# Kernel optimization log

Measured on AMD Instinct MI355X. Metric: run time of the kernel, lower is better.

The kernel has to match this reference:

```python
import jax, jax.numpy as jnp
import numpy as np

NUM_HEADS = 16


def setup_inputs() -> dict:
    key = jax.random.key(0)
    k1, k2, k3 = jax.random.split(key, 3)
    T, B, E = 2048, 2, 1024
    x = jax.random.normal(k1, (T, B, E), dtype=jnp.float32)
    in_proj_w = jax.random.normal(k2, (E, 3 * E), dtype=jnp.float32) * (E ** -0.5)
    in_proj_b = jnp.zeros((3 * E,), dtype=jnp.float32)
    out_w = jax.random.normal(k3, (E, E), dtype=jnp.float32) * (E ** -0.5)
    out_b = jnp.zeros((E,), dtype=jnp.float32)
    return {"x": x, "in_proj_w": in_proj_w, "in_proj_b": in_proj_b,
            "out_w": out_w, "out_b": out_b}


def reference(x, in_proj_w, in_proj_b, out_w, out_b):
    # x: (tgt_len, bsz, embed_dim) -- seq-first, self-attention (q is k is v)
    T, B, E = x.shape
    H = NUM_HEADS
    D = E // H
    scaling = D ** -0.5
    # packed in-projection: einsum('bne,ef->bnf') over (T,B,E)
    proj = jnp.einsum('tbe,ef->tbf', x, in_proj_w) + in_proj_b
    q, k, v = jnp.split(proj, 3, axis=-1)  # each (T, B, E)
    # reshape to (T, B*H, D) then transpose to (B*H, T, D)
    q = q.reshape(T, B * H, D).transpose(1, 0, 2)
    k = k.reshape(T, B * H, D).transpose(1, 0, 2)
    v = v.reshape(T, B * H, D).transpose(1, 0, 2)
    # full O(T^2) attention matrix, scaling applied after QK^T as in source
    attn = jnp.einsum('bie,bje->bij', q, k) * scaling  # (B*H, T, T)
    attn = jax.nn.softmax(attn, axis=-1)
    out = jnp.einsum('bij,bje->bie', attn, v)  # (B*H, T, D)
    # faithful to source: reshape directly (no head transpose-back)
    out = out.reshape(B, T, E)
    out = jnp.einsum('bte,ef->btf', out, out_w) + out_b
    return out
```

## Files before the change

### kernel.cpp

```cpp
#include <hip/hip_runtime.h>
#include <stdint.h>

#define TSEQ 2048
#define NB 2
#define EMB 1024
#define NHEAD 16
#define HDIM 64
#define KSPLIT 4
#define NT (TSEQ / KSPLIT / 64)
#define QSCALE 0.18033688f

typedef __bf16 bf16x8 __attribute__((ext_vector_type(8)));
typedef __bf16 bf16x4 __attribute__((ext_vector_type(4)));
typedef float f32x4 __attribute__((ext_vector_type(4)));

__device__ __forceinline__ void gload_lds16(const void* g, void* lds) {
    __builtin_amdgcn_global_load_lds(
        (const __attribute__((address_space(1))) unsigned int*)g,
        (__attribute__((address_space(3))) unsigned int*)lds, 16, 0, 0);
}

__global__ __launch_bounds__(256) void cvt_x_kernel(
    const float* __restrict__ x, __bf16* __restrict__ xb)
{
    const size_t idx = ((size_t)blockIdx.x * 256 + threadIdx.x) * 4;
    float4 v = *(const float4*)(x + idx);
    bf16x4 o = { (__bf16)v.x, (__bf16)v.y, (__bf16)v.z, (__bf16)v.w };
    *(bf16x4*)(xb + idx) = o;
}

__global__ __launch_bounds__(256) void transpose_cvt_kernel(
    const float* __restrict__ w_in, const float* __restrict__ w_out,
    __bf16* __restrict__ wiT, __bf16* __restrict__ whT)
{
    __shared__ float tile[32][33];
    int bx = blockIdx.x;
    const int by = blockIdx.y;
    const float* src; __bf16* dst; int sn;
    if (bx < 96) { src = w_in;  dst = wiT; sn = 3072; }
    else         { bx -= 96; src = w_out; dst = whT; sn = 1024; }
    const int tx = threadIdx.x, ty = threadIdx.y;
    #pragma unroll
    for (int i = 0; i < 4; ++i)
        tile[ty + i * 8][tx] = src[(size_t)(by * 32 + ty + i * 8) * sn + bx * 32 + tx];
    __syncthreads();
    #pragma unroll
    for (int i = 0; i < 4; ++i) {
        float v = tile[tx][ty + i * 8];
        dst[(size_t)(bx * 32 + ty + i * 8) * 1024 + by * 32 + tx] = (__bf16)v;
    }
}

__global__ __launch_bounds__(256) void gemm_qkv_kernel(
    const __bf16* __restrict__ A, const __bf16* __restrict__ BT,
    const float* __restrict__ bias,
    __bf16* __restrict__ Oq, __bf16* __restrict__ Ok, __bf16* __restrict__ Ov)
{
    __shared__ __align__(16) __bf16 As[128 * 64];
    __shared__ __align__(16) __bf16 Bs[128 * 64];
    const int tid = threadIdx.x;
    const int wave = tid >> 6, lane = tid & 63;
    const int l16 = lane & 15, quad = lane >> 4;
    const int wm = wave >> 1, wn = wave & 1;
    const int m0 = blockIdx.y * 128, n0 = blockIdx.x * 128;

    f32x4 acc[4][4];
    #pragma unroll
    for (int mt = 0; mt < 4; ++mt)
        #pragma unroll
        for (int nt = 0; nt < 4; ++nt)
            #pragma unroll
            for (int r = 0; r < 4; ++r) acc[mt][nt][r] = 0.f;

    int smrow[4], schunk[4], sbase[4];
    #pragma unroll
    for (int i = 0; i < 4; ++i) {
        int linear = (wave * 4 + i) * 64 + lane;
        smrow[i] = linear >> 3;
        schunk[i] = (linear & 7) ^ (smrow[i] & 7);
        sbase[i] = (wave * 4 + i) * 512;
    }

    for (int k0 = 0; k0 < 1024; k0 += 64) {
        #pragma unroll
        for (int i = 0; i < 4; ++i) {
            gload_lds16(A + (size_t)(m0 + smrow[i]) * 1024 + k0 + schunk[i] * 8,
                        As + sbase[i]);
            gload_lds16(BT + (size_t)(n0 + smrow[i]) * 1024 + k0 + schunk[i] * 8,
                        Bs + sbase[i]);
        }
        __syncthreads();
        #pragma unroll
        for (int kk = 0; kk < 2; ++kk) {
            bf16x8 am[4], bn[4];
            #pragma unroll
            for (int mt = 0; mt < 4; ++mt) {
                int row = wm * 64 + mt * 16 + l16;
                int c = (kk * 4 + quad) ^ (row & 7);
                am[mt] = *(const bf16x8*)(As + row * 64 + c * 8);
            }
            #pragma unroll
            for (int nt = 0; nt < 4; ++nt) {
                int row = wn * 64 + nt * 16 + l16;
                int c = (kk * 4 + quad) ^ (row & 7);
                bn[nt] = *(const bf16x8*)(Bs + row * 64 + c * 8);
            }
            #pragma unroll
            for (int mt = 0; mt < 4; ++mt)
                #pragma unroll
                for (int nt = 0; nt < 4; ++nt)
                    acc[mt][nt] = __builtin_amdgcn_mfma_f32_16x16x32_bf16(
                        am[mt], bn[nt], acc[mt][nt], 0, 0, 0);
        }
        __syncthreads();
    }

    #pragma unroll
    for (int nt = 0; nt < 4; ++nt) {
        const int col = n0 + wn * 64 + nt * 16 + l16;
        const float bv = bias[col];
        const int sec = col >> 10, f = col & 1023;
        const int h = f >> 6, d = f & 63;
        #pragma unroll
        for (int mt = 0; mt < 4; ++mt)
            #pragma unroll
            for (int r = 0; r < 4; ++r) {
                const int row = m0 + wm * 64 + mt * 16 + quad * 4 + r;
                float v = acc[mt][nt][r] + bv;
                const int t = row >> 1, b = row & 1;
                const int bh = b * NHEAD + h;
                if (sec == 0)
                    Oq[((size_t)bh * TSEQ + t) * HDIM + d] = (__bf16)(v * QSCALE);
                else if (sec == 1)
                    Ok[((size_t)bh * TSEQ + t) * HDIM + d] = (__bf16)v;
                else
                    Ov[((size_t)bh * HDIM + d) * TSEQ + t] = (__bf16)v;
            }
    }
}

__global__ __launch_bounds__(256, 4) void attn_mfma_kernel(
    const __bf16* __restrict__ Q, const __bf16* __restrict__ K,
    const __bf16* __restrict__ Vt,
    __bf16* __restrict__ O0, __bf16* __restrict__ O1,
    __bf16* __restrict__ O2, __bf16* __restrict__ O3,
    float* __restrict__ L0, float* __restrict__ L1,
    float* __restrict__ L2, float* __restrict__ L3)
{
    __shared__ __align__(16) __bf16 Ks[64 * 64];
    __shared__ __align__(16) __bf16 Vs[2][64 * 64];
    __shared__ __align__(16) __bf16 Ps[4][32 * 64];

    const int tid  = threadIdx.x;
    const int wave = tid >> 6;
    const int lane = tid & 63;
    const int l16  = lane & 15;
    const int quad = lane >> 4;
    const int bh   = blockIdx.y;
    const int z    = blockIdx.z;
    const int q0   = blockIdx.x * 128 + wave * 32;
    const int kbase0 = z * (TSEQ / KSPLIT);

    __bf16* __restrict__ Opart = (z == 0) ? O0 : (z == 1) ? O1 : (z == 2) ? O2 : O3;
    float*  __restrict__ Lpart = (z == 0) ? L0 : (z == 1) ? L1 : (z == 2) ? L2 : L3;

    bf16x8 qf[2][2];
    #pragma unroll
    for (int mq = 0; mq < 2; ++mq) {
        const __bf16* Qrow = Q + ((size_t)bh * TSEQ + q0 + mq * 16 + l16) * HDIM;
        qf[mq][0] = *(const bf16x8*)(Qrow + quad * 8);
        qf[mq][1] = *(const bf16x8*)(Qrow + 32 + quad * 8);
    }

    f32x4 Oacc[2][4];
    #pragma unroll
    for (int mq = 0; mq < 2; ++mq)
        #pragma unroll
        for (int dt = 0; dt < 4; ++dt)
            #pragma unroll
            for (int r = 0; r < 4; ++r) Oacc[mq][dt][r] = 0.f;
    float l_part[2] = {0.f, 0.f};

    const __bf16* Kbase = K + ((size_t)bh * TSEQ + kbase0) * HDIM;
    const __bf16* Vbase = Vt + (size_t)bh * HDIM * TSEQ + kbase0;

    int srow[2], schk[2];
    #pragma unroll
    for (int i = 0; i < 2; ++i) {
        const int s = wave * 2 + i;
        srow[i] = s * 8 + (lane >> 3);
        schk[i] = (lane & 7) ^ (srow[i] & 7);
    }

#define STAGE(buf, kt)                                                        \
    {                                                                         \
        _Pragma("unroll")                                                     \
        for (int i = 0; i < 2; ++i) {                                         \
            const int s = wave * 2 + i;                                       \
            gload_lds16(Kbase + (size_t)((kt) * 64 + srow[i]) * HDIM          \
                            + schk[i] * 8,                                    \
                        Ks + s * 512);                                        \
            gload_lds16(Vbase + (size_t)srow[i] * TSEQ + (kt) * 64            \
                            + schk[i] * 8,                                    \
                        &Vs[buf][s * 512]);                                   \
        }                                                                     \
    }

    STAGE(0, 0);

    for (int kt = 0; kt < NT; ++kt) {
        const int buf = kt & 1;
        __syncthreads();

        bf16x8 kf[4][2];
        #pragma unroll
        for (int nt = 0; nt < 4; ++nt) {
            const int row = nt * 16 + l16;
            #pragma unroll
            for (int ch = 0; ch < 2; ++ch) {
                const int c = (quad + 4 * ch) ^ (row & 7);
                kf[nt][ch] = *(const bf16x8*)(&Ks[row * 64 + c * 8]);
            }
        }
        __syncthreads();
        if (kt + 1 < NT) STAGE(buf ^ 1, kt + 1);

        #pragma unroll
        for (int mq = 0; mq < 2; ++mq) {
            #pragma unroll
            for (int nt = 0; nt < 4; ++nt) {
                f32x4 s = {0.f, 0.f, 0.f, 0.f};
                s = __builtin_amdgcn_mfma_f32_16x16x32_bf16(kf[nt][0], qf[mq][0], s, 0, 0, 0);
                s = __builtin_amdgcn_mfma_f32_16x16x32_bf16(kf[nt][1], qf[mq][1], s, 0, 0, 0);
                float p0 = exp2f(s[0]), p1 = exp2f(s[1]);
                float p2 = exp2f(s[2]), p3 = exp2f(s[3]);
                l_part[mq] += (p0 + p1) + (p2 + p3);
                bf16x4 pk = { (__bf16)p0, (__bf16)p1, (__bf16)p2, (__bf16)p3 };
                const int prow = mq * 16 + l16;
                const int kidx = nt * 16 + quad * 4;
                const int pos = ((kidx >> 3) ^ (prow & 7)) * 8 + (kidx & 7);
                *(bf16x4*)(&Ps[wave][prow * 64 + pos]) = pk;
            }
        }

        bf16x8 pa[2][2];
        #pragma unroll
        for (int mq = 0; mq < 2; ++mq) {
            const int prow = mq * 16 + l16;
            #pragma unroll
            for (int h = 0; h < 2; ++h) {
                const int c = (quad + 4 * h) ^ (prow & 7);
                pa[mq][h] = *(const bf16x8*)(&Ps[wave][prow * 64 + c * 8]);
            }
        }
        #pragma unroll
        for (int dt = 0; dt < 4; ++dt) {
            const int row = dt * 16 + l16;
            bf16x8 v0, v1;
            {
                const int c0 = quad ^ (row & 7);
                const int c1 = (quad + 4) ^ (row & 7);
                v0 = *(const bf16x8*)(&Vs[buf][row * 64 + c0 * 8]);
                v1 = *(const bf16x8*)(&Vs[buf][row * 64 + c1 * 8]);
            }
            #pragma unroll
            for (int mq = 0; mq < 2; ++mq) {
                Oacc[mq][dt] = __builtin_amdgcn_mfma_f32_16x16x32_bf16(
                    pa[mq][0], v0, Oacc[mq][dt], 0, 0, 0);
                Oacc[mq][dt] = __builtin_amdgcn_mfma_f32_16x16x32_bf16(
                    pa[mq][1], v1, Oacc[mq][dt], 0, 0, 0);
            }
        }
    }
#undef STAGE

    #pragma unroll
    for (int mq = 0; mq < 2; ++mq) {
        float v = l_part[mq];
        v += __shfl_xor(v, 16);
        v += __shfl_xor(v, 32);
        if (quad == 0)
            Lpart[(size_t)bh * TSEQ + q0 + mq * 16 + l16] = v;
    }

    const size_t base = ((size_t)bh * TSEQ + q0) * HDIM;
    #pragma unroll
    for (int mq = 0; mq < 2; ++mq)
        #pragma unroll
        for (int dt = 0; dt < 4; ++dt)
            #pragma unroll
            for (int r = 0; r < 4; ++r) {
                const size_t idx = base +
                    (size_t)(mq * 16 + quad * 4 + r) * HDIM + dt * 16 + l16;
                Opart[idx] = (__bf16)Oacc[mq][dt][r];
            }
}

__global__ __launch_bounds__(256) void normalize_kernel(
    const __bf16* __restrict__ O0, const __bf16* __restrict__ O1,
    const __bf16* __restrict__ O2, const __bf16* __restrict__ O3,
    const float* __restrict__ L0, const float* __restrict__ L1,
    const float* __restrict__ L2, const float* __restrict__ L3,
    __bf16* __restrict__ Ob)
{
    const size_t gid = (size_t)blockIdx.x * 256 + threadIdx.x;
    const size_t idx = gid * 8;
    const size_t qi = idx >> 6;
    const float inv = 1.f / (L0[qi] + L1[qi] + L2[qi] + L3[qi]);
    bf16x8 a = *(const bf16x8*)(O0 + idx);
    bf16x8 b = *(const bf16x8*)(O1 + idx);
    bf16x8 c = *(const bf16x8*)(O2 + idx);
    bf16x8 d = *(const bf16x8*)(O3 + idx);
    bf16x8 o;
    #pragma unroll
    for (int j = 0; j < 8; ++j)
        o[j] = (__bf16)((((float)a[j] + (float)b[j]) +
                         ((float)c[j] + (float)d[j])) * inv);
    *(bf16x8*)(Ob + idx) = o;
}

__global__ __launch_bounds__(256) void gemm_out_kernel(
    const __bf16* __restrict__ A, const __bf16* __restrict__ BT,
    const float* __restrict__ bias, float* __restrict__ out)
{
    __shared__ __align__(16) __bf16 As[64 * 64];
    __shared__ __align__(16) __bf16 Bs[64 * 64];
    const int tid = threadIdx.x;
    const int wave = tid >> 6, lane = tid & 63;
    const int l16 = lane & 15, quad = lane >> 4;
    const int wm = wave >> 1, wn = wave & 1;
    const int m0 = blockIdx.y * 64, n0 = blockIdx.x * 64;

    f32x4 acc[2][2];
    #pragma unroll
    for (int mt = 0; mt < 2; ++mt)
        #pragma unroll
        for (int nt = 0; nt < 2; ++nt)
            #pragma unroll
            for (int r = 0; r < 4; ++r) acc[mt][nt][r] = 0.f;

    int srow[2], schk[2], sbase[2];
    #pragma unroll
    for (int i = 0; i < 2; ++i) {
        const int s = wave * 2 + i;
        srow[i] = s * 8 + (lane >> 3);
        schk[i] = (lane & 7) ^ (srow[i] & 7);
        sbase[i] = s * 512;
    }

    for (int k0 = 0; k0 < 1024; k0 += 64) {
        #pragma unroll
        for (int i = 0; i < 2; ++i) {
            gload_lds16(A + (size_t)(m0 + srow[i]) * 1024 + k0 + schk[i] * 8,
                        As + sbase[i]);
            gload_lds16(BT + (size_t)(n0 + srow[i]) * 1024 + k0 + schk[i] * 8,
                        Bs + sbase[i]);
        }
        __syncthreads();
        #pragma unroll
        for (int kk = 0; kk < 2; ++kk) {
            bf16x8 am[2], bn[2];
            #pragma unroll
            for (int mt = 0; mt < 2; ++mt) {
                int row = wm * 32 + mt * 16 + l16;
                int c = (kk * 4 + quad) ^ (row & 7);
                am[mt] = *(const bf16x8*)(As + row * 64 + c * 8);
            }
            #pragma unroll
            for (int nt = 0; nt < 2; ++nt) {
                int row = wn * 32 + nt * 16 + l16;
                int c = (kk * 4 + quad) ^ (row & 7);
                bn[nt] = *(const bf16x8*)(Bs + row * 64 + c * 8);
            }
            #pragma unroll
            for (int mt = 0; mt < 2; ++mt)
                #pragma unroll
                for (int nt = 0; nt < 2; ++nt)
                    acc[mt][nt] = __builtin_amdgcn_mfma_f32_16x16x32_bf16(
                        am[mt], bn[nt], acc[mt][nt], 0, 0, 0);
        }
        __syncthreads();
    }

    #pragma unroll
    for (int nt = 0; nt < 2; ++nt) {
        const int col = n0 + wn * 32 + nt * 16 + l16;
        const float bv = bias[col];
        #pragma unroll
        for (int mt = 0; mt < 2; ++mt)
            #pragma unroll
            for (int r = 0; r < 4; ++r) {
                const int row = m0 + wm * 32 + mt * 16 + quad * 4 + r;
                out[(size_t)row * 1024 + col] = acc[mt][nt][r] + bv;
            }
    }
}

extern "C" void kernel_launch(void* const* d_in, const int* in_sizes, int n_in,
                              void* d_out, int out_size, void* d_ws, size_t ws_size,
                              hipStream_t stream) {
    const float* x     = (const float*)d_in[0];
    const float* w_in  = (const float*)d_in[1];
    const float* b_in  = (const float*)d_in[2];
    const float* w_out = (const float*)d_in[3];
    const float* b_out = (const float*)d_in[4];
    float* out = (float*)d_out;

    const size_t M1 = (size_t)1024 * 1024;
    __bf16* ws  = (__bf16*)d_ws;
    __bf16* xb  = ws;
    __bf16* wiT = xb  + 4 * M1;
    __bf16* whT = wiT + 3 * M1;
    __bf16* Qb  = whT + 1 * M1;
    __bf16* Kb  = Qb  + 4 * M1;
    __bf16* Vt  = Kb  + 4 * M1;
    __bf16* O0  = Vt  + 4 * M1;
    __bf16* O1  = O0  + 4 * M1;
    float*  L0  = (float*)(O1 + 4 * M1);
    float*  L1  = L0 + 65536;
    float*  L2  = L1 + 65536;
    float*  L3  = L2 + 65536;
    __bf16* O2  = (__bf16*)d_out;
    __bf16* O3  = O2 + 4 * M1;
    __bf16* Ob  = xb;

    cvt_x_kernel<<<4096, 256, 0, stream>>>(x, xb);
    transpose_cvt_kernel<<<dim3(128, 32), dim3(32, 8), 0, stream>>>(
        w_in, w_out, wiT, whT);
    gemm_qkv_kernel<<<dim3(24, 32), 256, 0, stream>>>(
        xb, wiT, b_in, Qb, Kb, Vt);
    attn_mfma_kernel<<<dim3(16, 32, KSPLIT), 256, 0, stream>>>(
        Qb, Kb, Vt, O0, O1, O2, O3, L0, L1, L2, L3);
    normalize_kernel<<<2048, 256, 0, stream>>>(
        O0, O1, O2, O3, L0, L1, L2, L3, Ob);
    gemm_out_kernel<<<dim3(16, 64), 256, 0, stream>>>(
        Ob, whT, b_out, out);
}
```

Baseline: 217.3 us.

## Write V row-major from QKV GEMM and transpose it in a separate kernel

The QKV GEMM epilogue now writes V in the same [bh][t][d] layout as Q and K. A new LDS-tiled kernel transposes it into Vt, replacing the strided scattered stores of the old transposed write. The attention kernel also shrinks its per-wave P scratch to 16 rows, interleaving the P write and read per query tile, which lowers LDS use. The cost is an extra kernel launch plus a V round trip through memory, using d_out as temporary storage.

```diff
diff --git a/kernel.cpp b/kernel.cpp
--- a/kernel.cpp
+++ b/kernel.cpp
@@ -129,14 +129,46 @@
                 float v = acc[mt][nt][r] + bv;
                 const int t = row >> 1, b = row & 1;
                 const int bh = b * NHEAD + h;
+                const size_t idx = ((size_t)bh * TSEQ + t) * HDIM + d;
                 if (sec == 0)
-                    Oq[((size_t)bh * TSEQ + t) * HDIM + d] = (__bf16)(v * QSCALE);
+                    Oq[idx] = (__bf16)(v * QSCALE);
                 else if (sec == 1)
-                    Ok[((size_t)bh * TSEQ + t) * HDIM + d] = (__bf16)v;
+                    Ok[idx] = (__bf16)v;
                 else
-                    Ov[((size_t)bh * HDIM + d) * TSEQ + t] = (__bf16)v;
-            }
-    }
+                    Ov[idx] = (__bf16)v;
+            }
+    }
+}
+
+__global__ __launch_bounds__(256) void vtrans_kernel(
+    const __bf16* __restrict__ V, __bf16* __restrict__ Vt)
+{
+    __shared__ __bf16 T[64 * 67];
+    const int bh = blockIdx.y;
+    const int t0 = blockIdx.x * 64;
+    const int tid = threadIdx.x;
+    const int r = tid >> 2;
+    const int c = (tid & 3) * 16;
+    const __bf16* src = V + ((size_t)bh * TSEQ + t0 + r) * HDIM + c;
+    bf16x8 a = *(const bf16x8*)src;
+    bf16x8 b = *(const bf16x8*)(src + 8);
+    #pragma unroll
+    for (int j = 0; j < 8; ++j) {
+        T[r * 67 + c + j] = a[j];
+        T[r * 67 + c + 8 + j] = b[j];
+    }
+    __syncthreads();
+    const int dr = tid >> 2;
+    const int tc = (tid & 3) * 16;
+    bf16x8 o0, o1;
+    #pragma unroll
+    for (int j = 0; j < 8; ++j) {
+        o0[j] = T[(tc + j) * 67 + dr];
+        o1[j] = T[(tc + 8 + j) * 67 + dr];
+    }
+    __bf16* dst = Vt + ((size_t)bh * HDIM + dr) * TSEQ + t0 + tc;
+    *(bf16x8*)dst = o0;
+    *(bf16x8*)(dst + 8) = o1;
 }
 
 __global__ __launch_bounds__(256, 4) void attn_mfma_kernel(
@@ -149,7 +181,7 @@
 {
     __shared__ __align__(16) __bf16 Ks[64 * 64];
     __shared__ __align__(16) __bf16 Vs[2][64 * 64];
-    __shared__ __align__(16) __bf16 Ps[4][32 * 64];
+    __shared__ __align__(16) __bf16 Ps[4][16 * 64];
 
     const int tid  = threadIdx.x;
     const int wave = tid >> 6;
@@ -225,6 +257,7 @@
         __syncthreads();
         if (kt + 1 < NT) STAGE(buf ^ 1, kt + 1);
 
+        bf16x8 pa[2][2];
         #pragma unroll
         for (int mq = 0; mq < 2; ++mq) {
             #pragma unroll
@@ -236,33 +269,24 @@
                 float p2 = exp2f(s[2]), p3 = exp2f(s[3]);
                 l_part[mq] += (p0 + p1) + (p2 + p3);
                 bf16x4 pk = { (__bf16)p0, (__bf16)p1, (__bf16)p2, (__bf16)p3 };
-                const int prow = mq * 16 + l16;
                 const int kidx = nt * 16 + quad * 4;
-                const int pos = ((kidx >> 3) ^ (prow & 7)) * 8 + (kidx & 7);
-                *(bf16x4*)(&Ps[wave][prow * 64 + pos]) = pk;
-            }
-        }
-
-        bf16x8 pa[2][2];
-        #pragma unroll
-        for (int mq = 0; mq < 2; ++mq) {
-            const int prow = mq * 16 + l16;
+                const int pos = ((kidx >> 3) ^ (l16 & 7)) * 8 + (kidx & 7);
+                *(bf16x4*)(&Ps[wave][l16 * 64 + pos]) = pk;
+            }
             #pragma unroll
             for (int h = 0; h < 2; ++h) {
-                const int c = (quad + 4 * h) ^ (prow & 7);
-                pa[mq][h] = *(const bf16x8*)(&Ps[wave][prow * 64 + c * 8]);
-            }
-        }
+                const int c = (quad + 4 * h) ^ (l16 & 7);
+                pa[mq][h] = *(const bf16x8*)(&Ps[wave][l16 * 64 + c * 8]);
+            }
+        }
+
         #pragma unroll
         for (int dt = 0; dt < 4; ++dt) {
             const int row = dt * 16 + l16;
-            bf16x8 v0, v1;
-            {
-                const int c0 = quad ^ (row & 7);
-                const int c1 = (quad + 4) ^ (row & 7);
-                v0 = *(const bf16x8*)(&Vs[buf][row * 64 + c0 * 8]);
-                v1 = *(const bf16x8*)(&Vs[buf][row * 64 + c1 * 8]);
-            }
+            const int c0 = quad ^ (row & 7);
+            const int c1 = (quad + 4) ^ (row & 7);
+            bf16x8 v0 = *(const bf16x8*)(&Vs[buf][row * 64 + c0 * 8]);
+            bf16x8 v1 = *(const bf16x8*)(&Vs[buf][row * 64 + c1 * 8]);
             #pragma unroll
             for (int mq = 0; mq < 2; ++mq) {
                 Oacc[mq][dt] = __builtin_amdgcn_mfma_f32_16x16x32_bf16(
@@ -420,6 +444,7 @@
     float*  L1  = L0 + 65536;
     float*  L2  = L1 + 65536;
     float*  L3  = L2 + 65536;
+    __bf16* Vb  = (__bf16*)d_out;
     __bf16* O2  = (__bf16*)d_out;
     __bf16* O3  = O2 + 4 * M1;
     __bf16* Ob  = xb;
@@ -428,7 +453,8 @@
     transpose_cvt_kernel<<<dim3(128, 32), dim3(32, 8), 0, stream>>>(
         w_in, w_out, wiT, whT);
     gemm_qkv_kernel<<<dim3(24, 32), 256, 0, stream>>>(
-        xb, wiT, b_in, Qb, Kb, Vt);
+        xb, wiT, b_in, Qb, Kb, Vb);
+    vtrans_kernel<<<dim3(32, 32), 256, 0, stream>>>(Vb, Vt);
     attn_mfma_kernel<<<dim3(16, 32, KSPLIT), 256, 0, stream>>>(
         Qb, Kb, Vt, O0, O1, O2, O3, L0, L1, L2, L3);
     normalize_kernel<<<2048, 256, 0, stream>>>(
```

After: 208.3 us. -4.2%, faster.
